# Kernel tuning notes

Hardware: AMD Instinct MI355X
Metric: run time of the kernel (lower is better)

The kernel has to match this reference:

```python
import jax, jax.numpy as jnp
import numpy as np

H = 50  # LSTM hidden size (fixed in source)


def setup_inputs() -> dict:
    key = jax.random.key(0)
    ks = jax.random.split(key, 8)
    B, T, P = 1024, 1024, 16
    s = 1.0 / np.sqrt(H)  # torch LSTM/Linear default init scale
    return {
        "x": jax.random.normal(ks[0], (B, T, 1), dtype=jnp.float32),
        "params": jax.random.normal(ks[1], (B, T, P), dtype=jnp.float32),
        "W_ih": jax.random.uniform(ks[2], (4 * H, 1), dtype=jnp.float32, minval=-s, maxval=s),
        "W_hh": jax.random.uniform(ks[3], (4 * H, H), dtype=jnp.float32, minval=-s, maxval=s),
        "b_ih": jax.random.uniform(ks[4], (4 * H,), dtype=jnp.float32, minval=-s, maxval=s),
        "b_hh": jax.random.uniform(ks[5], (4 * H,), dtype=jnp.float32, minval=-s, maxval=s),
        "W_lin": jax.random.uniform(ks[6], (1, H + P), dtype=jnp.float32, minval=-s, maxval=s),
        "b_lin": jax.random.uniform(ks[7], (1,), dtype=jnp.float32, minval=-s, maxval=s),
    }


def _lstm(x, W_ih, W_hh, b_ih, b_hh):
    # x: [B, T, 1] -> hidden sequence [B, T, H]. PyTorch gate order: i, f, g, o.
    B = x.shape[0]
    # Precompute input contribution for all timesteps: [B, T, 4H]
    xg = jnp.einsum('bti,gi->btg', x, W_ih) + b_ih + b_hh
    xg_t = jnp.swapaxes(xg, 0, 1)  # [T, B, 4H]

    def step(carry, g_in):
        h, c = carry
        gates = g_in + h @ W_hh.T  # [B, 4H]
        i, f, g, o = jnp.split(gates, 4, axis=-1)
        c = jax.nn.sigmoid(f) * c + jax.nn.sigmoid(i) * jnp.tanh(g)
        h = jax.nn.sigmoid(o) * jnp.tanh(c)
        return (h, c), h

    h0 = jnp.zeros((B, H), dtype=x.dtype)
    c0 = jnp.zeros((B, H), dtype=x.dtype)
    (_, _), hs = jax.lax.scan(step, (h0, c0), xg_t)
    return jnp.swapaxes(hs, 0, 1)  # [B, T, H]


def reference(x, params, W_ih, W_hh, b_ih, b_hh, W_lin, b_lin):
    hs = _lstm(x, W_ih, W_hh, b_ih, b_hh)            # [B, T, H]
    combined = jnp.concatenate((hs, params), axis=2)  # [B, T, H+P]
    return jnp.einsum('btf,of->bto', combined, W_lin) + b_lin  # [B, T, 1]
```

## Files before the change

kernel.cpp:

```cpp
#include <hip/hip_runtime.h>

namespace {

constexpr int Bn = 1024;
constexpr int Tn = 1024;
constexpr int Hn = 50;
constexpr int Pn = 16;
constexpr int KP = 25;

typedef _Float16 h2 __attribute__((ext_vector_type(2)));

__device__ __forceinline__ float fast_rcp(float x) { return __builtin_amdgcn_rcpf(x); }
__device__ __forceinline__ float fast_sigmoid(float x) {
    return fast_rcp(1.0f + __expf(-x));
}
__device__ __forceinline__ float fast_tanh(float x) {
    return 1.0f - 2.0f * fast_rcp(__expf(2.0f * x) + 1.0f);
}
__device__ __forceinline__ float fdot2(h2 a, h2 b, float c) {
    return __builtin_amdgcn_fdot2(a, b, c, false);
}

__global__ __launch_bounds__(256)
void params_proj(const float* __restrict__ params, const float* __restrict__ W_lin,
                 float* __restrict__ pp)
{
    const int i = blockIdx.x * 256 + threadIdx.x;
    const float4* p4 = (const float4*)(params + (size_t)i * Pn);
    const float4 a = p4[0], b = p4[1], c = p4[2], d = p4[3];
    const float* wl = W_lin + Hn;
    float s;
    s  = a.x * wl[ 0] + a.y * wl[ 1] + a.z * wl[ 2] + a.w * wl[ 3];
    s += b.x * wl[ 4] + b.y * wl[ 5] + b.z * wl[ 6] + b.w * wl[ 7];
    s += c.x * wl[ 8] + c.y * wl[ 9] + c.z * wl[10] + c.w * wl[11];
    s += d.x * wl[12] + d.y * wl[13] + d.z * wl[14] + d.w * wl[15];
    pp[i] = s;
}

__global__ __attribute__((amdgpu_flat_work_group_size(64, 64), amdgpu_waves_per_eu(1, 1)))
void lstm_core(const float* __restrict__ x, const float* __restrict__ W_ih,
               const float* __restrict__ W_hh, const float* __restrict__ b_ih,
               const float* __restrict__ b_hh, const float* __restrict__ W_lin,
               const float* __restrict__ b_lin, const float* __restrict__ pp,
               float* __restrict__ out)
{
    const int b    = blockIdx.x;
    const int lane = threadIdx.x;
    const int jj   = (lane < Hn) ? lane : Hn - 1;

    h2 w0[KP], w1[KP], w2[KP], w3[KP], wl[KP];
    const float* r0 = W_hh + (size_t)(0 * Hn + jj) * Hn;
    const float* r1 = W_hh + (size_t)(1 * Hn + jj) * Hn;
    const float* r2 = W_hh + (size_t)(2 * Hn + jj) * Hn;
    const float* r3 = W_hh + (size_t)(3 * Hn + jj) * Hn;
    #pragma unroll
    for (int k = 0; k < KP; ++k) {
        w0[k] = h2{(_Float16)r0[2 * k], (_Float16)r0[2 * k + 1]};
        w1[k] = h2{(_Float16)r1[2 * k], (_Float16)r1[2 * k + 1]};
        w2[k] = h2{(_Float16)r2[2 * k], (_Float16)r2[2 * k + 1]};
        w3[k] = h2{(_Float16)r3[2 * k], (_Float16)r3[2 * k + 1]};
        wl[k] = h2{(_Float16)W_lin[2 * k], (_Float16)W_lin[2 * k + 1]};
    }
    #pragma unroll
    for (int k = 0; k < KP; ++k) {
        asm volatile("" : "+v"(w0[k]), "+v"(w1[k]), "+v"(w2[k]), "+v"(w3[k]), "+v"(wl[k]));
    }

    const float wih0 = W_ih[0 * Hn + jj];
    const float wih1 = W_ih[1 * Hn + jj];
    const float wih2 = W_ih[2 * Hn + jj];
    const float wih3 = W_ih[3 * Hn + jj];
    const float bb0 = b_ih[0 * Hn + jj] + b_hh[0 * Hn + jj];
    const float bb1 = b_ih[1 * Hn + jj] + b_hh[1 * Hn + jj];
    const float bb2 = b_ih[2 * Hn + jj] + b_hh[2 * Hn + jj];
    const float bb3 = b_ih[3 * Hn + jj] + b_hh[3 * Hn + jj];
    const float blin = b_lin[0];

    const float4* xb4 = (const float4*)(x + (size_t)b * Tn);
    const float4* pp4 = (const float4*)(pp + (size_t)b * Tn);
    float4* ob4 = (float4*)(out + (size_t)b * Tn);

    float h = 0.0f, c = 0.0f;
    int sp[KP];
    #pragma unroll
    for (int k = 0; k < KP; ++k) sp[k] = 0;

    float4 xA = xb4[0], pA = pp4[0];

    for (int tt = 0; tt < Tn / 4; ++tt) {
        float4 xB = make_float4(0.f, 0.f, 0.f, 0.f), pB = xB;
        if (tt + 1 < Tn / 4) { xB = xb4[tt + 1]; pB = pp4[tt + 1]; }

        const float xs[4] = {xA.x, xA.y, xA.z, xA.w};
        const float ps[4] = {pA.x, pA.y, pA.z, pA.w};
        float o4[4];

        #pragma unroll
        for (int u = 0; u < 4; ++u) {
            float a0 = fmaf(xs[u], wih0, bb0);
            float a1 = fmaf(xs[u], wih1, bb1);
            float a2 = fmaf(xs[u], wih2, bb2);
            float a3 = fmaf(xs[u], wih3, bb3);
            #pragma unroll
            for (int k = 0; k < KP; ++k) {
                const h2 hp = __builtin_bit_cast(h2, sp[k]);
                a0 = fdot2(hp, w0[k], a0);
                a1 = fdot2(hp, w1[k], a1);
                a2 = fdot2(hp, w2[k], a2);
                a3 = fdot2(hp, w3[k], a3);
            }

            const float ig = fast_sigmoid(a0);
            const float fg = fast_sigmoid(a1);
            const float gg = fast_tanh(a2);
            const float og = fast_sigmoid(a3);
            c = fmaf(fg, c, ig * gg);
            h = og * fast_tanh(c);

            const int hi = __builtin_bit_cast(int, h);
            const int hj = __builtin_amdgcn_update_dpp(0, hi, 0xB1, 0xF, 0xF, true);
            const int packed = __builtin_bit_cast(int,
                __builtin_amdgcn_cvt_pkrtz(h, __builtin_bit_cast(float, hj)));

            #pragma unroll
            for (int k = 0; k < KP; ++k)
                sp[k] = __builtin_amdgcn_readlane(packed, 2 * k);

            float prj = ps[u] + blin;
            #pragma unroll
            for (int k = 0; k < KP; ++k)
                prj = fdot2(__builtin_bit_cast(h2, sp[k]), wl[k], prj);
            o4[u] = prj;
        }

        if (lane == 0) ob4[tt] = make_float4(o4[0], o4[1], o4[2], o4[3]);
        xA = xB; pA = pB;
    }
}

}

extern "C" void kernel_launch(void* const* d_in, const int* in_sizes, int n_in,
                              void* d_out, int out_size, void* d_ws, size_t ws_size,
                              hipStream_t stream) {
    const float* x      = (const float*)d_in[0];
    const float* params = (const float*)d_in[1];
    const float* W_ih   = (const float*)d_in[2];
    const float* W_hh   = (const float*)d_in[3];
    const float* b_ih   = (const float*)d_in[4];
    const float* b_hh   = (const float*)d_in[5];
    const float* W_lin  = (const float*)d_in[6];
    const float* b_lin  = (const float*)d_in[7];
    float* out = (float*)d_out;
    float* pp  = (float*)d_ws;

    params_proj<<<dim3(Bn * Tn / 256), dim3(256), 0, stream>>>(params, W_lin, pp);
    lstm_core<<<dim3(Bn), dim3(64), 0, stream>>>(
        x, W_ih, W_hh, b_ih, b_hh, W_lin, b_lin, pp, out);
}
```

Measured before the change: 588.7 us.

## Split output projection out of serial LSTM loop into parallel post-pass

Result: faster. 488.3 us (-17.1%).

```diff
diff --git a/kernel.cpp b/kernel.cpp
--- a/kernel.cpp
+++ b/kernel.cpp
@@ -1,4 +1,5 @@
 #include <hip/hip_runtime.h>
+#include <stdint.h>
 
 namespace {
 
@@ -19,6 +20,123 @@
 }
 __device__ __forceinline__ float fdot2(h2 a, h2 b, float c) {
     return __builtin_amdgcn_fdot2(a, b, c, false);
+}
+
+__global__ __attribute__((amdgpu_flat_work_group_size(64, 64), amdgpu_waves_per_eu(1, 1)))
+void lstm_core_h(const float* __restrict__ x, const float* __restrict__ W_ih,
+                 const float* __restrict__ W_hh, const float* __restrict__ b_ih,
+                 const float* __restrict__ b_hh, uint32_t* __restrict__ hbuf)
+{
+    const int b    = blockIdx.x;
+    const int lane = threadIdx.x;
+    const int jj   = (lane < Hn) ? lane : Hn - 1;
+
+    h2 w0[KP], w1[KP], w2[KP], w3[KP];
+    const float* r0 = W_hh + (size_t)(0 * Hn + jj) * Hn;
+    const float* r1 = W_hh + (size_t)(1 * Hn + jj) * Hn;
+    const float* r2 = W_hh + (size_t)(2 * Hn + jj) * Hn;
+    const float* r3 = W_hh + (size_t)(3 * Hn + jj) * Hn;
+    #pragma unroll
+    for (int k = 0; k < KP; ++k) {
+        w0[k] = h2{(_Float16)r0[2 * k], (_Float16)r0[2 * k + 1]};
+        w1[k] = h2{(_Float16)r1[2 * k], (_Float16)r1[2 * k + 1]};
+        w2[k] = h2{(_Float16)r2[2 * k], (_Float16)r2[2 * k + 1]};
+        w3[k] = h2{(_Float16)r3[2 * k], (_Float16)r3[2 * k + 1]};
+    }
+    #pragma unroll
+    for (int k = 0; k < KP; ++k) {
+        asm volatile("" : "+v"(w0[k]), "+v"(w1[k]), "+v"(w2[k]), "+v"(w3[k]));
+    }
+
+    const float wih0 = W_ih[0 * Hn + jj];
+    const float wih1 = W_ih[1 * Hn + jj];
+    const float wih2 = W_ih[2 * Hn + jj];
+    const float wih3 = W_ih[3 * Hn + jj];
+    const float bb0 = b_ih[0 * Hn + jj] + b_hh[0 * Hn + jj];
+    const float bb1 = b_ih[1 * Hn + jj] + b_hh[1 * Hn + jj];
+    const float bb2 = b_ih[2 * Hn + jj] + b_hh[2 * Hn + jj];
+    const float bb3 = b_ih[3 * Hn + jj] + b_hh[3 * Hn + jj];
+
+    const float4* xb4 = (const float4*)(x + (size_t)b * Tn);
+
+    uint32_t* hb = hbuf + ((size_t)b * KP + (size_t)(lane >> 1)) * Tn;
+    const bool writer = (lane < Hn) && ((lane & 1) == 0);
+
+    float h = 0.0f, c = 0.0f;
+    int sp[KP];
+    #pragma unroll
+    for (int k = 0; k < KP; ++k) sp[k] = 0;
+
+    float4 xA = xb4[0];
+
+    for (int tt = 0; tt < Tn / 4; ++tt) {
+        float4 xB = make_float4(0.f, 0.f, 0.f, 0.f);
+        if (tt + 1 < Tn / 4) xB = xb4[tt + 1];
+
+        const float xs[4] = {xA.x, xA.y, xA.z, xA.w};
+
+        #pragma unroll
+        for (int u = 0; u < 4; ++u) {
+            float a0 = fmaf(xs[u], wih0, bb0);
+            float a1 = fmaf(xs[u], wih1, bb1);
+            float a2 = fmaf(xs[u], wih2, bb2);
+            float a3 = fmaf(xs[u], wih3, bb3);
+            #pragma unroll
+            for (int k = 0; k < KP; ++k) {
+                const h2 hp = __builtin_bit_cast(h2, sp[k]);
+                a0 = fdot2(hp, w0[k], a0);
+                a1 = fdot2(hp, w1[k], a1);
+                a2 = fdot2(hp, w2[k], a2);
+                a3 = fdot2(hp, w3[k], a3);
+            }
+
+            const float ig = fast_sigmoid(a0);
+            const float fg = fast_sigmoid(a1);
+            const float gg = fast_tanh(a2);
+            const float og = fast_sigmoid(a3);
+            c = fmaf(fg, c, ig * gg);
+            h = og * fast_tanh(c);
+
+            const int hi = __builtin_bit_cast(int, h);
+            const int hj = __builtin_amdgcn_update_dpp(0, hi, 0xB1, 0xF, 0xF, true);
+            const int packed = __builtin_bit_cast(int,
+                __builtin_amdgcn_cvt_pkrtz(h, __builtin_bit_cast(float, hj)));
+
+            if (writer) hb[tt * 4 + u] = (uint32_t)packed;
+
+            #pragma unroll
+            for (int k = 0; k < KP; ++k)
+                sp[k] = __builtin_amdgcn_readlane(packed, 2 * k);
+        }
+        xA = xB;
+    }
+}
+
+__global__ __launch_bounds__(256)
+void post_proj(const uint32_t* __restrict__ hbuf, const float* __restrict__ params,
+               const float* __restrict__ W_lin, const float* __restrict__ b_lin,
+               float* __restrict__ out)
+{
+    const int i = blockIdx.x * 256 + threadIdx.x;
+    const int b = i >> 10;
+    const int t = i & (Tn - 1);
+
+    float s = b_lin[0];
+    const uint32_t* hp = hbuf + (size_t)b * KP * Tn + t;
+    #pragma unroll
+    for (int k = 0; k < KP; ++k) {
+        const h2 wlk = h2{(_Float16)W_lin[2 * k], (_Float16)W_lin[2 * k + 1]};
+        s = fdot2(__builtin_bit_cast(h2, hp[(size_t)k * Tn]), wlk, s);
+    }
+
+    const float4* p4 = (const float4*)(params + (size_t)i * Pn);
+    const float4 a = p4[0], bq = p4[1], cq = p4[2], dq = p4[3];
+    const float* wp = W_lin + Hn;
+    s += a.x  * wp[ 0] + a.y  * wp[ 1] + a.z  * wp[ 2] + a.w  * wp[ 3];
+    s += bq.x * wp[ 4] + bq.y * wp[ 5] + bq.z * wp[ 6] + bq.w * wp[ 7];
+    s += cq.x * wp[ 8] + cq.y * wp[ 9] + cq.z * wp[10] + cq.w * wp[11];
+    s += dq.x * wp[12] + dq.y * wp[13] + dq.z * wp[14] + dq.w * wp[15];
+    out[i] = s;
 }
 
 __global__ __launch_bounds__(256)
@@ -38,11 +156,11 @@
 }
 
 __global__ __attribute__((amdgpu_flat_work_group_size(64, 64), amdgpu_waves_per_eu(1, 1)))
-void lstm_core(const float* __restrict__ x, const float* __restrict__ W_ih,
-               const float* __restrict__ W_hh, const float* __restrict__ b_ih,
-               const float* __restrict__ b_hh, const float* __restrict__ W_lin,
-               const float* __restrict__ b_lin, const float* __restrict__ pp,
-               float* __restrict__ out)
+void lstm_core_fused(const float* __restrict__ x, const float* __restrict__ W_ih,
+                     const float* __restrict__ W_hh, const float* __restrict__ b_ih,
+                     const float* __restrict__ b_hh, const float* __restrict__ W_lin,
+                     const float* __restrict__ b_lin, const float* __restrict__ pp,
+                     float* __restrict__ out)
 {
     const int b    = blockIdx.x;
     const int lane = threadIdx.x;
@@ -152,9 +270,19 @@
     const float* W_lin  = (const float*)d_in[6];
     const float* b_lin  = (const float*)d_in[7];
     float* out = (float*)d_out;
-    float* pp  = (float*)d_ws;
-
-    params_proj<<<dim3(Bn * Tn / 256), dim3(256), 0, stream>>>(params, W_lin, pp);
-    lstm_core<<<dim3(Bn), dim3(64), 0, stream>>>(
-        x, W_ih, W_hh, b_ih, b_hh, W_lin, b_lin, pp, out);
-}
+
+    const size_t hbuf_bytes = (size_t)Bn * KP * Tn * sizeof(uint32_t);
+
+    if (ws_size >= hbuf_bytes) {
+        uint32_t* hbuf = (uint32_t*)d_ws;
+        lstm_core_h<<<dim3(Bn), dim3(64), 0, stream>>>(
+            x, W_ih, W_hh, b_ih, b_hh, hbuf);
+        post_proj<<<dim3(Bn * Tn / 256), dim3(256), 0, stream>>>(
+            hbuf, params, W_lin, b_lin, out);
+    } else {
+        float* pp = (float*)d_ws;
+        params_proj<<<dim3(Bn * Tn / 256), dim3(256), 0, stream>>>(params, W_lin, pp);
+        lstm_core_fused<<<dim3(Bn), dim3(64), 0, stream>>>(
+            x, W_ih, W_hh, b_ih, b_hh, W_lin, b_lin, pp, out);
+    }
+}
```
